# Kernel optimization log

Hardware: AMD Instinct MI355X
Metric: run time of the kernel (lower is better)

Reference implementation:

```python
import jax, jax.numpy as jnp
import numpy as np

EPS = 1e-8

def setup_inputs() -> dict:
    key = jax.random.key(0)
    k0, k1, k2, k3, k4 = jax.random.split(key, 5)
    B, N, K, Q, L, F = 8, 5, 5, 4, 128, 768
    support_emb = jax.random.normal(k0, (B, N, K, L, F), dtype=jnp.float32)
    query_emb = jax.random.normal(k1, (B, N * Q, L, F), dtype=jnp.float32)
    B_mask = jax.random.randint(k2, (B, N, K, L), 0, 2, dtype=jnp.int32)
    I_mask = jax.random.randint(k3, (B, N, K, L), 0, 2, dtype=jnp.int32)
    trigger_label = jax.random.randint(k4, (B, N * Q, L), 0, 2 * N + 1, dtype=jnp.int32)
    return {"support_emb": support_emb, "query_emb": query_emb, "B_mask": B_mask,
            "I_mask": I_mask, "trigger_label": trigger_label, "N": N, "K": K, "Q": Q}

def _proto(support_emb, Bm, Im, N):
    # support_emb: (B,N,K,L,F); Bm/Im: (B,N,K,L) float
    sum_B = jnp.einsum('bnklf,bnkl->bnf', support_emb, Bm)
    cnt_B = Bm.sum((2, 3))[..., None] + EPS
    pB = sum_B / cnt_B                                   # (B,N,F)
    sum_I = jnp.einsum('bnklf,bnkl->bnf', support_emb, Im)
    cnt_I = Im.sum((2, 3))[..., None] + EPS
    pI = sum_I / cnt_I                                   # (B,N,F)
    Om = 1.0 - Bm - Im                                   # (B,N,K,L)
    sum_O = jnp.einsum('bnklf,bnkl->bf', support_emb, Om)
    cnt_O = Om.sum((1, 2, 3))[:, None] + EPS
    pO = sum_O / cnt_O                                   # (B,F)
    Bsz, F = pO.shape
    # interleave: tags [O, B_0, I_0, B_1, I_1, ...]
    pBI = jnp.stack([pB, pI], axis=2).reshape(Bsz, 2 * N, F)
    return jnp.concatenate([pO[:, None, :], pBI], axis=1)  # (B, 2N+1, F)

def reference(support_emb, query_emb, B_mask, I_mask, trigger_label, N, K, Q):
    dt = support_emb.dtype
    Bm = B_mask.astype(dt)
    Im = I_mask.astype(dt)
    prototype = _proto(support_emb, Bm, Im, N)             # (B, 2N+1, F)
    # similarity: broadcast dot product -> batched GEMM
    logits = jnp.einsum('bqlf,btf->bqlt', query_emb, prototype)  # (B, NQ, L, 2N+1)
    T = logits.shape[-1]
    flat = logits.reshape(-1, T)
    pred = jnp.argmax(flat, axis=1)
    lab = trigger_label.reshape(-1)
    logp = jax.nn.log_softmax(flat, axis=-1)
    loss = -jnp.take_along_axis(logp, lab[:, None], axis=1).mean()
    return (loss, logits, pred)
```

## Files before the change

### kernel.cpp

```cpp
#include <hip/hip_runtime.h>
#include <cstdint>
#include <cstddef>

#define EPS 1e-8f

#define Bsz 8
#define Nn  5
#define Kk  5
#define Ll  128
#define Ff  768
#define Tt  11
#define KL  640
#define ROWS_PER_B 2560
#define NROWS 20480
#define F4  192
#define BN  40

#define S1_ROWS 64
#define S1_G    4
#define S1_GR   16
#define S1_CH   (KL / S1_ROWS)
#define S1_NBLK (BN * S1_CH)
#define PART_STRIDE (3 * Ff)
#define PART_STRIDE4 (PART_STRIDE / 4)

typedef float v2f __attribute__((ext_vector_type(2)));

__global__ __launch_bounds__(768) void stage1(
    const float* __restrict__ sup,
    const int*   __restrict__ Bm,
    const int*   __restrict__ Im,
    float* __restrict__ part,
    float* __restrict__ pcnt)
{
    __shared__ float4 red[S1_G * 3 * F4];
    __shared__ float  redc[S1_G * 2];

    int blk = blockIdx.x;
    int bn  = blk / S1_CH;
    int ch  = blk - bn * S1_CH;
    int tid = threadIdx.x;
    int g   = tid / 192;
    int col = tid - g * 192;
    int rbase = ch * S1_ROWS + g * S1_GR;

    const float4* sp = (const float4*)(sup + ((size_t)bn * KL + rbase) * Ff) + col;
    const int*    bp = Bm + bn * KL + rbase;
    const int*    ip = Im + bn * KL + rbase;

    v2f tB0 = {0.f,0.f}, tB1 = tB0, tI0 = tB0, tI1 = tB0, tA0 = tB0, tA1 = tB0;
    int cB = 0, cI = 0;

    #pragma unroll
    for (int h = 0; h < S1_GR / 8; ++h) {
        float4 v[8];
        #pragma unroll
        for (int j = 0; j < 8; ++j) v[j] = sp[(size_t)(h * 8 + j) * F4];
        #pragma unroll
        for (int j = 0; j < 8; ++j) {
            int p = h * 8 + j;
            v2f lo = {v[j].x, v[j].y};
            v2f hi = {v[j].z, v[j].w};
            tA0 += lo; tA1 += hi;
            if (bp[p]) { tB0 += lo; tB1 += hi; ++cB; }
            if (ip[p]) { tI0 += lo; tI1 += hi; ++cI; }
        }
    }

    red[(g * 3 + 0) * F4 + col] = (float4){tB0.x, tB0.y, tB1.x, tB1.y};
    red[(g * 3 + 1) * F4 + col] = (float4){tI0.x, tI0.y, tI1.x, tI1.y};
    red[(g * 3 + 2) * F4 + col] = (float4){tA0.x, tA0.y, tA1.x, tA1.y};
    if (col == 0) { redc[g * 2] = (float)cB; redc[g * 2 + 1] = (float)cI; }
    __syncthreads();

    if (tid < 3 * F4) {
        int set = tid / F4;
        int c   = tid - set * F4;
        float4 a = red[(0 * 3 + set) * F4 + c];
        float4 b = red[(1 * 3 + set) * F4 + c];
        float4 d = red[(2 * 3 + set) * F4 + c];
        float4 e = red[(3 * 3 + set) * F4 + c];
        float4 s = {a.x + b.x + d.x + e.x, a.y + b.y + d.y + e.y,
                    a.z + b.z + d.z + e.z, a.w + b.w + d.w + e.w};
        ((float4*)(part + (size_t)blk * PART_STRIDE))[tid] = s;
    }
    if (tid == 0) {
        pcnt[2 * (size_t)blk]     = redc[0] + redc[2] + redc[4] + redc[6];
        pcnt[2 * (size_t)blk + 1] = redc[1] + redc[3] + redc[5] + redc[7];
    }
}

#define S2_Q  4
#define S2_QF (F4 / S2_Q)

__global__ __launch_bounds__(512) void stage2f(
    const float* __restrict__ part,
    const float* __restrict__ pcnt,
    float* __restrict__ proto,
    float* __restrict__ loss_out)
{
    __shared__ float4 bns[Nn * 3 * S2_QF];
    __shared__ float  scnt[2 * Nn];

    int blk = blockIdx.x;
    int b   = blk / S2_Q;
    int q   = blk - b * S2_Q;
    int tid = threadIdx.x;

    if (blk == 0 && tid == 0) loss_out[0] = 0.0f;

    for (int it = tid; it < Nn * 3 * S2_QF; it += 512) {
        int n   = it / (3 * S2_QF);
        int r   = it - n * (3 * S2_QF);
        int set = r / S2_QF;
        int f   = r - set * S2_QF;
        const float4* src = (const float4*)part
            + ((size_t)((b * Nn + n) * S1_CH) * 3 + set) * F4 + (q * S2_QF + f);
        float4 s = {0, 0, 0, 0};
        float4 v[S1_CH];
        #pragma unroll
        for (int c = 0; c < S1_CH; ++c) v[c] = src[(size_t)c * PART_STRIDE4];
        #pragma unroll
        for (int c = 0; c < S1_CH; ++c) {
            s.x += v[c].x; s.y += v[c].y; s.z += v[c].z; s.w += v[c].w;
        }
        bns[it] = s;
    }
    if (tid < 2 * Nn) {
        int n = tid >> 1, set = tid & 1;
        float cv = 0.0f;
        #pragma unroll
        for (int c = 0; c < S1_CH; ++c)
            cv += pcnt[2 * ((size_t)(b * Nn + n) * S1_CH + c) + set];
        scnt[tid] = cv;
    }
    __syncthreads();

    for (int it = tid; it < Tt * S2_QF; it += 512) {
        int t = it / S2_QF;
        int f = it - t * S2_QF;
        float scale;
        float4 val;
        if (t == 0) {
            float cO = (float)(KL * Nn);
            #pragma unroll
            for (int k = 0; k < 2 * Nn; ++k) cO -= scnt[k];
            scale = 1.0f / (cO + EPS);
            float sx = 0, sy = 0, sz = 0, sw = 0;
            #pragma unroll
            for (int n = 0; n < Nn; ++n) {
                float4 A  = bns[(n * 3 + 2) * S2_QF + f];
                float4 Bv = bns[(n * 3 + 0) * S2_QF + f];
                float4 Iv = bns[(n * 3 + 1) * S2_QF + f];
                sx += A.x - Bv.x - Iv.x; sy += A.y - Bv.y - Iv.y;
                sz += A.z - Bv.z - Iv.z; sw += A.w - Bv.w - Iv.w;
            }
            val = (float4){sx, sy, sz, sw};
        } else {
            int n  = (t - 1) >> 1;
            int st = (t - 1) & 1;
            scale = 1.0f / (scnt[t - 1] + EPS);
            val = bns[(n * 3 + st) * S2_QF + f];
        }
        val.x *= scale; val.y *= scale; val.z *= scale; val.w *= scale;
        ((float4*)proto)[((size_t)b * Tt + t) * F4 + q * S2_QF + f] = val;
    }
}

#define S3_ROWS 64
#define S3_NBLK (NROWS / S3_ROWS)

__global__ __launch_bounds__(128) void stage3(
    const float* __restrict__ query,
    const float* __restrict__ proto,
    const int*   __restrict__ label,
    float* __restrict__ out_logits,
    float* __restrict__ out_pred,
    float* __restrict__ loss_out)
{
    __shared__ float4 ldsP[Tt * F4];
    __shared__ float  lred[2];

    int blk = blockIdx.x;
    int tid = threadIdx.x;
    int b   = blk / (ROWS_PER_B / S3_ROWS);

    const float4* pp = (const float4*)proto + (size_t)b * Tt * F4;
    for (int idx = tid; idx < Tt * F4; idx += 128) ldsP[idx] = pp[idx];
    __syncthreads();

    int p = tid >> 4;
    int s = tid & 15;

    size_t row0 = (size_t)blk * S3_ROWS + p * 8;
    const float4* qb = (const float4*)query + row0 * F4 + s;

    float a[8][Tt];
    #pragma unroll
    for (int r = 0; r < 8; ++r)
        #pragma unroll
        for (int t = 0; t < Tt; ++t) a[r][t] = 0.0f;

    float4 u[8], w[8];
    #pragma unroll
    for (int r = 0; r < 8; ++r) u[r] = qb[r * F4];

    const float4* pb = ldsP + s;
    for (int jj = 0; jj < 6; ++jj) {
        int j0 = 2 * jj, j1 = 2 * jj + 1;
        #pragma unroll
        for (int r = 0; r < 8; ++r) w[r] = qb[r * F4 + j1 * 16];
        #pragma unroll
        for (int t = 0; t < Tt; ++t) {
            float4 pv = pb[t * F4 + j0 * 16];
            #pragma unroll
            for (int r = 0; r < 8; ++r) {
                float d = a[r][t];
                d = fmaf(u[r].x, pv.x, d); d = fmaf(u[r].y, pv.y, d);
                d = fmaf(u[r].z, pv.z, d); d = fmaf(u[r].w, pv.w, d);
                a[r][t] = d;
            }
        }
        int o2 = (jj < 5) ? (2 * jj + 2) * 16 : 0;
        #pragma unroll
        for (int r = 0; r < 8; ++r) u[r] = qb[r * F4 + o2];
        #pragma unroll
        for (int t = 0; t < Tt; ++t) {
            float4 pv = pb[t * F4 + j1 * 16];
            #pragma unroll
            for (int r = 0; r < 8; ++r) {
                float d = a[r][t];
                d = fmaf(w[r].x, pv.x, d); d = fmaf(w[r].y, pv.y, d);
                d = fmaf(w[r].z, pv.z, d); d = fmaf(w[r].w, pv.w, d);
                a[r][t] = d;
            }
        }
    }

    #pragma unroll
    for (int r = 0; r < 8; ++r)
        #pragma unroll
        for (int t = 0; t < Tt; ++t) {
            float v = a[r][t];
            v += __shfl_xor(v, 1, 16); v += __shfl_xor(v, 2, 16);
            v += __shfl_xor(v, 4, 16); v += __shfl_xor(v, 8, 16);
            a[r][t] = v;
        }

    float wloss = 0.0f;
    if (s < 8) {
        float rv[Tt];
        #pragma unroll
        for (int t = 0; t < Tt; ++t)
            rv[t] = (s == 0) ? a[0][t] : (s == 1) ? a[1][t] : (s == 2) ? a[2][t]
                  : (s == 3) ? a[3][t] : (s == 4) ? a[4][t] : (s == 5) ? a[5][t]
                  : (s == 6) ? a[6][t] : a[7][t];
        size_t grow = row0 + s;

        float m = rv[0]; int bt = 0;
        #pragma unroll
        for (int t = 1; t < Tt; ++t) if (rv[t] > m) { m = rv[t]; bt = t; }
        float sum = 0.0f;
        #pragma unroll
        for (int t = 0; t < Tt; ++t) sum += __expf(rv[t] - m);
        int lab = label[grow];
        float labv = rv[0];
        #pragma unroll
        for (int t = 1; t < Tt; ++t) labv = (lab == t) ? rv[t] : labv;
        #pragma unroll
        for (int t = 0; t < Tt; ++t) out_logits[grow * Tt + t] = rv[t];
        out_pred[grow] = (float)bt;
        wloss = (m + __logf(sum)) - labv;
    }
    #pragma unroll
    for (int off = 32; off > 0; off >>= 1) wloss += __shfl_xor(wloss, off, 64);
    if ((tid & 63) == 0) lred[tid >> 6] = wloss;
    __syncthreads();
    if (tid == 0)
        atomicAdd(loss_out, (lred[0] + lred[1]) * (1.0f / (float)NROWS));
}

extern "C" void kernel_launch(void* const* d_in, const int* in_sizes, int n_in,
                              void* d_out, int out_size, void* d_ws, size_t ws_size,
                              hipStream_t stream) {
    const float* sup   = (const float*)d_in[0];
    const float* query = (const float*)d_in[1];
    const int*   Bm    = (const int*)d_in[2];
    const int*   Im    = (const int*)d_in[3];
    const int*   lab   = (const int*)d_in[4];

    float* w     = (float*)d_ws;
    float* part  = w;
    float* pcnt  = part + (size_t)S1_NBLK * PART_STRIDE;
    float* proto = pcnt + 2 * S1_NBLK;

    float* loss_out   = (float*)d_out;
    float* out_logits = (float*)d_out + 1;
    float* out_pred   = (float*)d_out + 1 + (size_t)NROWS * Tt;

    stage1<<<S1_NBLK, 768, 0, stream>>>(sup, Bm, Im, part, pcnt);
    stage2f<<<Bsz * S2_Q, 512, 0, stream>>>(part, pcnt, proto, loss_out);
    stage3<<<S3_NBLK, 128, 0, stream>>>(query, proto, lab,
                                        out_logits, out_pred, loss_out);
}
```

Baseline: 195.5 us.

## Replace two-stage prototype reduction with atomic accumulation and fold finalize into GEMM stage

Stage1 now runs as 256 blocks that each stream a contiguous run of support rows and atomically add per-class partial sums and counts into a zeroed workspace, which removes the separate stage2 reduction kernel. The prototype scaling and the O-tag combination move into the prologue of stage3, which each block recomputes from the class sums. Stage3 also goes to 256 threads with 80 rows per block and 10 rows per 32-lane group. In exchange the code adds a zeroing kernel, float atomics whose summation order is nondeterministic, redundant prototype work in every stage3 block, and higher register pressure.

```diff
diff --git a/kernel.cpp b/kernel.cpp
--- a/kernel.cpp
+++ b/kernel.cpp
@@ -15,220 +15,188 @@
 #define NROWS 20480
 #define F4  192
 #define BN  40
-
-#define S1_ROWS 64
-#define S1_G    4
-#define S1_GR   16
-#define S1_CH   (KL / S1_ROWS)
-#define S1_NBLK (BN * S1_CH)
-#define PART_STRIDE (3 * Ff)
-#define PART_STRIDE4 (PART_STRIDE / 4)
+#define SUP_ROWS (BN * KL)
 
 typedef float v2f __attribute__((ext_vector_type(2)));
 
-__global__ __launch_bounds__(768) void stage1(
+__global__ __launch_bounds__(256) void zerok(float4* __restrict__ z,
+                                             float* __restrict__ loss_out)
+{
+    int gid = blockIdx.x * 256 + threadIdx.x;
+    if (gid == 0) loss_out[0] = 0.0f;
+    if (gid < (BN * 3 * Ff + 2 * BN) / 4) z[gid] = (float4){0.f, 0.f, 0.f, 0.f};
+}
+
+__global__ __launch_bounds__(192) void stage1p(
     const float* __restrict__ sup,
     const int*   __restrict__ Bm,
     const int*   __restrict__ Im,
-    float* __restrict__ part,
-    float* __restrict__ pcnt)
+    float* __restrict__ bnsum,
+    float* __restrict__ cnt)
 {
-    __shared__ float4 red[S1_G * 3 * F4];
-    __shared__ float  redc[S1_G * 2];
-
     int blk = blockIdx.x;
-    int bn  = blk / S1_CH;
-    int ch  = blk - bn * S1_CH;
     int tid = threadIdx.x;
-    int g   = tid / 192;
-    int col = tid - g * 192;
-    int rbase = ch * S1_ROWS + g * S1_GR;
-
-    const float4* sp = (const float4*)(sup + ((size_t)bn * KL + rbase) * Ff) + col;
-    const int*    bp = Bm + bn * KL + rbase;
-    const int*    ip = Im + bn * KL + rbase;
-
-    v2f tB0 = {0.f,0.f}, tB1 = tB0, tI0 = tB0, tI1 = tB0, tA0 = tB0, tA1 = tB0;
-    int cB = 0, cI = 0;
-
-    #pragma unroll
-    for (int h = 0; h < S1_GR / 8; ++h) {
-        float4 v[8];
-        #pragma unroll
-        for (int j = 0; j < 8; ++j) v[j] = sp[(size_t)(h * 8 + j) * F4];
-        #pragma unroll
-        for (int j = 0; j < 8; ++j) {
-            int p = h * 8 + j;
-            v2f lo = {v[j].x, v[j].y};
-            v2f hi = {v[j].z, v[j].w};
-            tA0 += lo; tA1 += hi;
-            if (bp[p]) { tB0 += lo; tB1 += hi; ++cB; }
-            if (ip[p]) { tI0 += lo; tI1 += hi; ++cI; }
-        }
-    }
-
-    red[(g * 3 + 0) * F4 + col] = (float4){tB0.x, tB0.y, tB1.x, tB1.y};
-    red[(g * 3 + 1) * F4 + col] = (float4){tI0.x, tI0.y, tI1.x, tI1.y};
-    red[(g * 3 + 2) * F4 + col] = (float4){tA0.x, tA0.y, tA1.x, tA1.y};
-    if (col == 0) { redc[g * 2] = (float)cB; redc[g * 2 + 1] = (float)cI; }
-    __syncthreads();
-
-    if (tid < 3 * F4) {
-        int set = tid / F4;
-        int c   = tid - set * F4;
-        float4 a = red[(0 * 3 + set) * F4 + c];
-        float4 b = red[(1 * 3 + set) * F4 + c];
-        float4 d = red[(2 * 3 + set) * F4 + c];
-        float4 e = red[(3 * 3 + set) * F4 + c];
-        float4 s = {a.x + b.x + d.x + e.x, a.y + b.y + d.y + e.y,
-                    a.z + b.z + d.z + e.z, a.w + b.w + d.w + e.w};
-        ((float4*)(part + (size_t)blk * PART_STRIDE))[tid] = s;
-    }
-    if (tid == 0) {
-        pcnt[2 * (size_t)blk]     = redc[0] + redc[2] + redc[4] + redc[6];
-        pcnt[2 * (size_t)blk + 1] = redc[1] + redc[3] + redc[5] + redc[7];
-    }
-}
-
-#define S2_Q  4
-#define S2_QF (F4 / S2_Q)
-
-__global__ __launch_bounds__(512) void stage2f(
-    const float* __restrict__ part,
-    const float* __restrict__ pcnt,
-    float* __restrict__ proto,
-    float* __restrict__ loss_out)
-{
-    __shared__ float4 bns[Nn * 3 * S2_QF];
-    __shared__ float  scnt[2 * Nn];
-
-    int blk = blockIdx.x;
-    int b   = blk / S2_Q;
-    int q   = blk - b * S2_Q;
-    int tid = threadIdx.x;
-
-    if (blk == 0 && tid == 0) loss_out[0] = 0.0f;
-
-    for (int it = tid; it < Nn * 3 * S2_QF; it += 512) {
-        int n   = it / (3 * S2_QF);
-        int r   = it - n * (3 * S2_QF);
-        int set = r / S2_QF;
-        int f   = r - set * S2_QF;
-        const float4* src = (const float4*)part
-            + ((size_t)((b * Nn + n) * S1_CH) * 3 + set) * F4 + (q * S2_QF + f);
-        float4 s = {0, 0, 0, 0};
-        float4 v[S1_CH];
-        #pragma unroll
-        for (int c = 0; c < S1_CH; ++c) v[c] = src[(size_t)c * PART_STRIDE4];
-        #pragma unroll
-        for (int c = 0; c < S1_CH; ++c) {
-            s.x += v[c].x; s.y += v[c].y; s.z += v[c].z; s.w += v[c].w;
-        }
-        bns[it] = s;
-    }
-    if (tid < 2 * Nn) {
-        int n = tid >> 1, set = tid & 1;
-        float cv = 0.0f;
-        #pragma unroll
-        for (int c = 0; c < S1_CH; ++c)
-            cv += pcnt[2 * ((size_t)(b * Nn + n) * S1_CH + c) + set];
-        scnt[tid] = cv;
-    }
-    __syncthreads();
-
-    for (int it = tid; it < Tt * S2_QF; it += 512) {
-        int t = it / S2_QF;
-        int f = it - t * S2_QF;
-        float scale;
-        float4 val;
-        if (t == 0) {
-            float cO = (float)(KL * Nn);
-            #pragma unroll
-            for (int k = 0; k < 2 * Nn; ++k) cO -= scnt[k];
-            scale = 1.0f / (cO + EPS);
-            float sx = 0, sy = 0, sz = 0, sw = 0;
-            #pragma unroll
-            for (int n = 0; n < Nn; ++n) {
-                float4 A  = bns[(n * 3 + 2) * S2_QF + f];
-                float4 Bv = bns[(n * 3 + 0) * S2_QF + f];
-                float4 Iv = bns[(n * 3 + 1) * S2_QF + f];
-                sx += A.x - Bv.x - Iv.x; sy += A.y - Bv.y - Iv.y;
-                sz += A.z - Bv.z - Iv.z; sw += A.w - Bv.w - Iv.w;
-            }
-            val = (float4){sx, sy, sz, sw};
-        } else {
-            int n  = (t - 1) >> 1;
-            int st = (t - 1) & 1;
-            scale = 1.0f / (scnt[t - 1] + EPS);
-            val = bns[(n * 3 + st) * S2_QF + f];
-        }
-        val.x *= scale; val.y *= scale; val.z *= scale; val.w *= scale;
-        ((float4*)proto)[((size_t)b * Tt + t) * F4 + q * S2_QF + f] = val;
-    }
-}
-
-#define S3_ROWS 64
+
+    int row = blk * (SUP_ROWS / 256);
+    const int row_end = row + (SUP_ROWS / 256);
+
+    while (row < row_end) {
+        int bn      = row / KL;
+        int seg_end = min(row_end, (bn + 1) * KL);
+        int len     = seg_end - row;
+
+        const float4* sp = (const float4*)sup + (size_t)row * F4 + tid;
+        const int*    bp = Bm + row;
+        const int*    ip = Im + row;
+
+        v2f tB0 = {0.f,0.f}, tB1 = tB0, tI0 = tB0, tI1 = tB0, tA0 = tB0, tA1 = tB0;
+        int cB = 0, cI = 0;
+
+        int r = 0;
+        for (; r + 8 <= len; r += 8) {
+            float4 v[8];
+            #pragma unroll
+            for (int j = 0; j < 8; ++j) v[j] = sp[(size_t)(r + j) * F4];
+            #pragma unroll
+            for (int j = 0; j < 8; ++j) {
+                v2f lo = {v[j].x, v[j].y};
+                v2f hi = {v[j].z, v[j].w};
+                tA0 += lo; tA1 += hi;
+                if (bp[r + j]) { tB0 += lo; tB1 += hi; ++cB; }
+                if (ip[r + j]) { tI0 += lo; tI1 += hi; ++cI; }
+            }
+        }
+        for (; r + 4 <= len; r += 4) {
+            float4 v[4];
+            #pragma unroll
+            for (int j = 0; j < 4; ++j) v[j] = sp[(size_t)(r + j) * F4];
+            #pragma unroll
+            for (int j = 0; j < 4; ++j) {
+                v2f lo = {v[j].x, v[j].y};
+                v2f hi = {v[j].z, v[j].w};
+                tA0 += lo; tA1 += hi;
+                if (bp[r + j]) { tB0 += lo; tB1 += hi; ++cB; }
+                if (ip[r + j]) { tI0 += lo; tI1 += hi; ++cI; }
+            }
+        }
+
+        float* dst = bnsum + (size_t)bn * (3 * Ff) + tid * 4;
+        atomicAdd(dst + 0,          tB0.x); atomicAdd(dst + 1,          tB0.y);
+        atomicAdd(dst + 2,          tB1.x); atomicAdd(dst + 3,          tB1.y);
+        atomicAdd(dst + Ff + 0,     tI0.x); atomicAdd(dst + Ff + 1,     tI0.y);
+        atomicAdd(dst + Ff + 2,     tI1.x); atomicAdd(dst + Ff + 3,     tI1.y);
+        atomicAdd(dst + 2 * Ff + 0, tA0.x); atomicAdd(dst + 2 * Ff + 1, tA0.y);
+        atomicAdd(dst + 2 * Ff + 2, tA1.x); atomicAdd(dst + 2 * Ff + 3, tA1.y);
+        if (tid == 0) {
+            atomicAdd(&cnt[2 * bn + 0], (float)cB);
+            atomicAdd(&cnt[2 * bn + 1], (float)cI);
+        }
+        row = seg_end;
+    }
+}
+
+#define S3_ROWS 80
 #define S3_NBLK (NROWS / S3_ROWS)
 
-__global__ __launch_bounds__(128) void stage3(
+__global__ __launch_bounds__(256, 1) void stage3(
     const float* __restrict__ query,
-    const float* __restrict__ proto,
+    const float* __restrict__ bnsum,
+    const float* __restrict__ cnt,
     const int*   __restrict__ label,
     float* __restrict__ out_logits,
     float* __restrict__ out_pred,
     float* __restrict__ loss_out)
 {
     __shared__ float4 ldsP[Tt * F4];
-    __shared__ float  lred[2];
+    __shared__ float  sCnt[2 * Nn];
+    __shared__ float  sScale[Tt];
+    __shared__ float  lred[4];
 
     int blk = blockIdx.x;
+    int b   = blk >> 5;
     int tid = threadIdx.x;
-    int b   = blk / (ROWS_PER_B / S3_ROWS);
-
-    const float4* pp = (const float4*)proto + (size_t)b * Tt * F4;
-    for (int idx = tid; idx < Tt * F4; idx += 128) ldsP[idx] = pp[idx];
-    __syncthreads();
-
-    int p = tid >> 4;
-    int s = tid & 15;
-
-    size_t row0 = (size_t)blk * S3_ROWS + p * 8;
+
+    if (tid < 2 * Nn) sCnt[tid] = cnt[2 * Nn * b + tid];
+    __syncthreads();
+    if (tid < Tt) {
+        if (tid == 0) {
+            float cO = (float)(KL * Nn);
+            #pragma unroll
+            for (int k = 0; k < 2 * Nn; ++k) cO -= sCnt[k];
+            sScale[0] = 1.0f / (cO + EPS);
+        } else {
+            sScale[tid] = 1.0f / (sCnt[tid - 1] + EPS);
+        }
+    }
+    __syncthreads();
+
+    const float4* bs = (const float4*)bnsum + (size_t)b * Nn * 3 * F4;
+    for (int idx = tid; idx < Tt * F4; idx += 256) {
+        int t  = idx / F4;
+        int f4 = idx - t * F4;
+        float4 val;
+        if (t == 0) {
+            float sx = 0, sy = 0, sz = 0, sw = 0;
+            #pragma unroll
+            for (int n = 0; n < Nn; ++n) {
+                float4 A  = bs[(n * 3 + 2) * F4 + f4];
+                float4 Bv = bs[(n * 3 + 0) * F4 + f4];
+                float4 Iv = bs[(n * 3 + 1) * F4 + f4];
+                sx += A.x - Bv.x - Iv.x; sy += A.y - Bv.y - Iv.y;
+                sz += A.z - Bv.z - Iv.z; sw += A.w - Bv.w - Iv.w;
+            }
+            val = (float4){sx, sy, sz, sw};
+        } else {
+            int n  = (t - 1) >> 1;
+            int st = (t - 1) & 1;
+            val = bs[(n * 3 + st) * F4 + f4];
+        }
+        float sc = sScale[t];
+        val.x *= sc; val.y *= sc; val.z *= sc; val.w *= sc;
+        ldsP[idx] = val;
+    }
+    __syncthreads();
+
+    int p = tid >> 5;
+    int s = tid & 31;
+
+    size_t row0 = (size_t)blk * S3_ROWS + p * 10;
     const float4* qb = (const float4*)query + row0 * F4 + s;
 
-    float a[8][Tt];
-    #pragma unroll
-    for (int r = 0; r < 8; ++r)
+    float a[10][Tt];
+    #pragma unroll
+    for (int r = 0; r < 10; ++r)
         #pragma unroll
         for (int t = 0; t < Tt; ++t) a[r][t] = 0.0f;
 
-    float4 u[8], w[8];
-    #pragma unroll
-    for (int r = 0; r < 8; ++r) u[r] = qb[r * F4];
+    float4 u[10], w[10];
+    #pragma unroll
+    for (int r = 0; r < 10; ++r) u[r] = qb[(size_t)r * F4];
 
     const float4* pb = ldsP + s;
-    for (int jj = 0; jj < 6; ++jj) {
+    for (int jj = 0; jj < 3; ++jj) {
         int j0 = 2 * jj, j1 = 2 * jj + 1;
         #pragma unroll
-        for (int r = 0; r < 8; ++r) w[r] = qb[r * F4 + j1 * 16];
+        for (int r = 0; r < 10; ++r) w[r] = qb[(size_t)r * F4 + (j0 + 1) * 32];
         #pragma unroll
         for (int t = 0; t < Tt; ++t) {
-            float4 pv = pb[t * F4 + j0 * 16];
-            #pragma unroll
-            for (int r = 0; r < 8; ++r) {
+            float4 pv = pb[t * F4 + j0 * 32];
+            #pragma unroll
+            for (int r = 0; r < 10; ++r) {
                 float d = a[r][t];
                 d = fmaf(u[r].x, pv.x, d); d = fmaf(u[r].y, pv.y, d);
                 d = fmaf(u[r].z, pv.z, d); d = fmaf(u[r].w, pv.w, d);
                 a[r][t] = d;
             }
         }
-        int o2 = (jj < 5) ? (2 * jj + 2) * 16 : 0;
-        #pragma unroll
-        for (int r = 0; r < 8; ++r) u[r] = qb[r * F4 + o2];
+        int o2 = (jj < 2) ? (j1 + 1) * 32 : 0;
+        #pragma unroll
+        for (int r = 0; r < 10; ++r) u[r] = qb[(size_t)r * F4 + o2];
         #pragma unroll
         for (int t = 0; t < Tt; ++t) {
-            float4 pv = pb[t * F4 + j1 * 16];
-            #pragma unroll
-            for (int r = 0; r < 8; ++r) {
+            float4 pv = pb[t * F4 + j1 * 32];
+            #pragma unroll
+            for (int r = 0; r < 10; ++r) {
                 float d = a[r][t];
                 d = fmaf(w[r].x, pv.x, d); d = fmaf(w[r].y, pv.y, d);
                 d = fmaf(w[r].z, pv.z, d); d = fmaf(w[r].w, pv.w, d);
@@ -238,23 +206,25 @@
     }
 
     #pragma unroll
-    for (int r = 0; r < 8; ++r)
+    for (int r = 0; r < 10; ++r)
         #pragma unroll
         for (int t = 0; t < Tt; ++t) {
             float v = a[r][t];
-            v += __shfl_xor(v, 1, 16); v += __shfl_xor(v, 2, 16);
-            v += __shfl_xor(v, 4, 16); v += __shfl_xor(v, 8, 16);
+            v += __shfl_xor(v, 1, 32);  v += __shfl_xor(v, 2, 32);
+            v += __shfl_xor(v, 4, 32);  v += __shfl_xor(v, 8, 32);
+            v += __shfl_xor(v, 16, 32);
             a[r][t] = v;
         }
 
     float wloss = 0.0f;
-    if (s < 8) {
+    if (s < 10) {
         float rv[Tt];
         #pragma unroll
         for (int t = 0; t < Tt; ++t)
             rv[t] = (s == 0) ? a[0][t] : (s == 1) ? a[1][t] : (s == 2) ? a[2][t]
                   : (s == 3) ? a[3][t] : (s == 4) ? a[4][t] : (s == 5) ? a[5][t]
-                  : (s == 6) ? a[6][t] : a[7][t];
+                  : (s == 6) ? a[6][t] : (s == 7) ? a[7][t] : (s == 8) ? a[8][t]
+                  : a[9][t];
         size_t grow = row0 + s;
 
         float m = rv[0]; int bt = 0;
@@ -277,7 +247,7 @@
     if ((tid & 63) == 0) lred[tid >> 6] = wloss;
     __syncthreads();
     if (tid == 0)
-        atomicAdd(loss_out, (lred[0] + lred[1]) * (1.0f / (float)NROWS));
+        atomicAdd(loss_out, (lred[0] + lred[1] + lred[2] + lred[3]) * (1.0f / (float)NROWS));
 }
 
 extern "C" void kernel_launch(void* const* d_in, const int* in_sizes, int n_in,
@@ -290,16 +260,15 @@
     const int*   lab   = (const int*)d_in[4];
 
     float* w     = (float*)d_ws;
-    float* part  = w;
-    float* pcnt  = part + (size_t)S1_NBLK * PART_STRIDE;
-    float* proto = pcnt + 2 * S1_NBLK;
+    float* bnsum = w;
+    float* cnt   = bnsum + (size_t)BN * 3 * Ff;
 
     float* loss_out   = (float*)d_out;
     float* out_logits = (float*)d_out + 1;
     float* out_pred   = (float*)d_out + 1 + (size_t)NROWS * Tt;
 
-    stage1<<<S1_NBLK, 768, 0, stream>>>(sup, Bm, Im, part, pcnt);
-    stage2f<<<Bsz * S2_Q, 512, 0, stream>>>(part, pcnt, proto, loss_out);
-    stage3<<<S3_NBLK, 128, 0, stream>>>(query, proto, lab,
+    zerok<<<91, 256, 0, stream>>>((float4*)w, loss_out);
+    stage1p<<<256, 192, 0, stream>>>(sup, Bm, Im, bnsum, cnt);
+    stage3<<<S3_NBLK, 256, 0, stream>>>(query, bnsum, cnt, lab,
                                         out_logits, out_pred, loss_out);
 }
```

Result: slower. 199.9 us (+2.2%).
